# Kernel optimization log

Measured on AMD Instinct MI355X. Metric: run time of the kernel, lower is better.

## Reference

```python
import jax, jax.numpy as jnp
import numpy as np

S = 128          # voxel grid resolution per axis
NPB = 50000      # active voxels per batch element
B = 2            # batch size
C_IN = 64
C_OUT = 64
K = 3            # kernel size

# kernel offsets in [-1,0,1]^3, shape [27, 3]
_OFFS = np.stack(np.meshgrid(np.arange(-1, 2), np.arange(-1, 2), np.arange(-1, 2), indexing='ij'), axis=-1).reshape(-1, 3)


def setup_inputs() -> dict:
    rng = np.random.default_rng(0)
    coords_list = []
    for b in range(B):
        lin = rng.choice(S * S * S, size=NPB, replace=False)  # unique voxels
        x = lin // (S * S)
        y = (lin // S) % S
        z = lin % S
        coords_list.append(np.stack([np.full(NPB, b), x, y, z], axis=1))
    coords = jnp.asarray(np.concatenate(coords_list, axis=0), dtype=jnp.int32)  # [N,4]

    key = jax.random.key(0)
    k1, k2, k3 = jax.random.split(key, 3)
    feats = jax.random.normal(k1, (B * NPB, C_IN), dtype=jnp.float32)
    fan1 = C_IN * K ** 3
    fan2 = C_OUT * K ** 3
    W1 = jax.random.normal(k2, (K ** 3, C_IN, C_OUT), dtype=jnp.float32) / np.sqrt(fan1)
    W2 = jax.random.normal(k3, (K ** 3, C_OUT, C_OUT), dtype=jnp.float32) / np.sqrt(fan2)
    return {"feats": feats, "coords": coords, "W1": W1, "W2": W2}


def _encode(coords):
    # linear key: ((b*S + x)*S + y)*S + z ; fits in int32 for S=128, B small
    b, x, y, z = coords[:, 0], coords[:, 1], coords[:, 2], coords[:, 3]
    return ((b * S + x) * S + y) * S + z


def _sparse_conv(feats, coords, W):
    """Stride-1 sparse (submanifold-style) 3D conv: output coords == input coords.
    feats [N,Cin], coords [N,4], W [27,Cin,Cout] -> [N,Cout]."""
    N = feats.shape[0]
    keys = _encode(coords)
    order = jnp.argsort(keys)
    skeys = keys[order]
    offs = jnp.asarray(_OFFS, dtype=jnp.int32)  # [27,3]

    def gather_one(d):
        qxyz = coords[:, 1:4] + d[None, :]
        valid = jnp.all((qxyz >= 0) & (qxyz < S), axis=1)
        qkey = keys + (d[0] * S * S + d[1] * S + d[2])
        idx = jnp.clip(jnp.searchsorted(skeys, qkey), 0, N - 1)
        found = valid & (skeys[idx] == qkey)
        return jnp.where(found[:, None], feats[order[idx]], 0.0)  # [N,Cin]

    gathered = jax.vmap(gather_one)(offs)  # [27, N, Cin]
    return jnp.einsum('onc,ocd->nd', gathered, W)


def reference(feats, coords, W1, W2):
    h = _sparse_conv(feats, coords, W1)
    out = _sparse_conv(h, coords, W2)
    return out
```

## Files before the change

### kernel.cpp

```cpp
#include <hip/hip_runtime.h>
#include <stdint.h>

#define SGRID 128
#define CAP 4096

typedef _Float16 f16;
typedef f16 f16x8 __attribute__((ext_vector_type(8)));
typedef float f32x4 __attribute__((ext_vector_type(4)));
typedef unsigned long long u64;

static __device__ __forceinline__ f32x4 mfma16(uint4 a, uint4 b, f32x4 c) {
    union { uint4 u; f16x8 v; } ua, ub;
    ua.u = a; ub.u = b;
    return __builtin_amdgcn_mfma_f32_16x16x32_f16(ua.v, ub.v, c, 0, 0, 0);
}

static __device__ __forceinline__ void split8(const float* v, uint4& hu, uint4& lu) {
    union { f16 h[8]; uint4 u; } hv, lv;
    #pragma unroll
    for (int j = 0; j < 8; ++j) {
        f16 h = (f16)v[j];
        hv.h[j] = h;
        lv.h[j] = (f16)(v[j] - (float)h);
    }
    hu = hv.u; lu = lv.u;
}

static __device__ __forceinline__ void center_body(
    const float* __restrict__ A, const f16* __restrict__ Wp,
    float* __restrict__ O, int N, int gw, int lane)
{
    const int r = lane & 15, lq = lane >> 4;
    const int p0 = gw * 32;

    const uint4* wb = (const uint4*)Wp + 13 * 512 + lane;
    uint4 b[2][4];
    #pragma unroll
    for (int ct = 0; ct < 4; ++ct)
        #pragma unroll
        for (int ks = 0; ks < 2; ++ks)
            b[ks][ct] = wb[(ct * 2 + ks) * 64];

    uint4 ah[2][2], al[2][2];
    #pragma unroll
    for (int rt = 0; rt < 2; ++rt) {
        int row = p0 + rt * 16 + r;
        #pragma unroll
        for (int ks = 0; ks < 2; ++ks) {
            float v[8];
            if (row < N) {
                float4 v0 = *(const float4*)(A + (size_t)row * 64 + ks * 32 + lq * 8);
                float4 v1 = *(const float4*)(A + (size_t)row * 64 + ks * 32 + lq * 8 + 4);
                v[0]=v0.x; v[1]=v0.y; v[2]=v0.z; v[3]=v0.w;
                v[4]=v1.x; v[5]=v1.y; v[6]=v1.z; v[7]=v1.w;
            } else {
                #pragma unroll
                for (int j = 0; j < 8; ++j) v[j] = 0.f;
            }
            split8(v, ah[rt][ks], al[rt][ks]);
        }
    }

    f32x4 acc[2][4];
    #pragma unroll
    for (int i = 0; i < 2; ++i)
        #pragma unroll
        for (int j = 0; j < 4; ++j) acc[i][j] = (f32x4){0.f, 0.f, 0.f, 0.f};

    #pragma unroll
    for (int ks = 0; ks < 2; ++ks)
        #pragma unroll
        for (int rt = 0; rt < 2; ++rt)
            #pragma unroll
            for (int ct = 0; ct < 4; ++ct) {
                acc[rt][ct] = mfma16(ah[rt][ks], b[ks][ct], acc[rt][ct]);
                acc[rt][ct] = mfma16(al[rt][ks], b[ks][ct], acc[rt][ct]);
            }

    #pragma unroll
    for (int rt = 0; rt < 2; ++rt)
        #pragma unroll
        for (int j = 0; j < 4; ++j) {
            int row = p0 + rt * 16 + lq * 4 + j;
            if (row < N) {
                #pragma unroll
                for (int ct = 0; ct < 4; ++ct)
                    O[(size_t)row * 64 + ct * 16 + r] = acc[rt][ct][j];
            }
        }
}

__global__ void clear_meta(uint4* __restrict__ bitmap4, int nwords4, int* __restrict__ cnt) {
    const int stride = gridDim.x * 256;
    for (int i = blockIdx.x * 256 + threadIdx.x; i < nwords4; i += stride)
        bitmap4[i] = (uint4){0, 0, 0, 0};
    if (blockIdx.x == 0 && threadIdx.x < 26) cnt[threadIdx.x * 16] = 0;
}

__global__ void __launch_bounds__(256) scatter_prep(
    const int* __restrict__ coords, int* __restrict__ table,
    unsigned* __restrict__ bitmap, int N, int scatB,
    const float* __restrict__ W1, const float* __restrict__ W2,
    f16* __restrict__ Wp1, f16* __restrict__ Wp2)
{
    const int tid = threadIdx.x;
    if (blockIdx.x < scatB) {
        int i = blockIdx.x * 256 + tid;
        if (i < N) {
            int4 c = ((const int4*)coords)[i];
            int key = ((c.x * SGRID + c.y) * SGRID + c.z) * SGRID + c.w;
            table[key] = i;
            atomicOr(&bitmap[key >> 5], 1u << (key & 31));
        }
        return;
    }
    int idx = (blockIdx.x - scatB) * 256 + tid;
    const int half = 27 * 512;
    const float* W = (idx < half) ? W1 : W2;
    f16* Wp = (idx < half) ? Wp1 : Wp2;
    int id = (idx < half) ? idx : idx - half;
    int lane = id & 63;
    int ks = (id >> 6) & 1;
    int ct = (id >> 7) & 3;
    int o  = id >> 9;
    int co  = ct * 16 + (lane & 15);
    int ci0 = ks * 32 + (lane >> 4) * 8;
    union { f16 h[8]; uint4 u; } hv;
    #pragma unroll
    for (int j = 0; j < 8; ++j)
        hv.h[j] = (f16)W[((size_t)o * 64 + ci0 + j) * 64 + co];
    ((uint4*)Wp)[id] = hv.u;
}

__global__ void __launch_bounds__(256) build(
    const int* __restrict__ coords, const int* __restrict__ table,
    const unsigned* __restrict__ bitmap,
    int* __restrict__ pin, int* __restrict__ pout, int* __restrict__ cnt, int N)
{
    __shared__ u64 sbal[26][4];
    __shared__ int sbase4[26][4];

    const int tid = threadIdx.x, lane = tid & 63, wave = tid >> 6;
    const int n = blockIdx.x * 256 + tid;
    const bool valid = n < N;

    int4 c = {0, 0, 0, 0};
    if (valid) c = ((const int4*)coords)[n];
    const int z  = c.w;
    const int zb = (z == 0) ? 0 : z - 1;
    const int wofs = zb >> 5, sh = zb & 31;

    unsigned omask = 0;
    #pragma unroll
    for (int cidx = 0; cidx < 9; ++cidx) {
        int dx = cidx / 3 - 1, dy = cidx % 3 - 1;
        int qx = c.y + dx, qy = c.z + dy;
        bool colok = valid && ((unsigned)qx < SGRID) && ((unsigned)qy < SGRID);
        int colbase = ((c.x * SGRID + qx) * SGRID + qy) << 2;
        int wi = colok ? (colbase + wofs) : 0;
        unsigned w0 = bitmap[wi];
        unsigned w1 = bitmap[wi + 1];
        u64 w = (u64)w0 | ((u64)w1 << 32);
        unsigned t = (unsigned)(w >> sh) & 7u;
        if (z == 0)         t = (t << 1) & 6u;
        if (z == SGRID - 1) t &= 3u;
        t = colok ? t : 0u;
        omask |= t << (cidx * 3);
    }
    omask &= ~(1u << 13);

    #pragma unroll
    for (int s = 0; s < 26; ++s) {
        int o = s < 13 ? s : s + 1;
        u64 bal = __ballot((omask >> o) & 1u);
        if (lane == 0) sbal[s][wave] = bal;
    }
    __syncthreads();

    if (tid < 26) {
        int c0 = (int)__popcll(sbal[tid][0]);
        int c1 = (int)__popcll(sbal[tid][1]);
        int c2 = (int)__popcll(sbal[tid][2]);
        int c3 = (int)__popcll(sbal[tid][3]);
        int tot = c0 + c1 + c2 + c3;
        int base = tot ? atomicAdd(&cnt[tid * 16], tot) : 0;
        sbase4[tid][0] = base;
        sbase4[tid][1] = base + c0;
        sbase4[tid][2] = base + c0 + c1;
        sbase4[tid][3] = base + c0 + c1 + c2;
    }
    __syncthreads();

    const int key = ((c.x * SGRID + c.y) * SGRID + c.z) * SGRID + z;
    const u64 ltmask = (1ull << lane) - 1ull;
    unsigned m = omask;
    while (m) {
        int o = __ffs(m) - 1;
        m &= m - 1;
        int s = o - (o > 13 ? 1 : 0);
        int dx = o / 9 - 1;
        int r9 = o - (dx + 1) * 9;
        int dy = r9 / 3 - 1;
        int dz = r9 - (dy + 1) * 3 - 1;
        int qkey = key + dx * SGRID * SGRID + dy * SGRID + dz;
        int v = table[qkey];
        int pos = sbase4[s][wave] + (int)__popcll(sbal[s][wave] & ltmask);
        if (pos < CAP) {
            pin[s * CAP + pos]  = v;
            pout[s * CAP + pos] = n;
        }
    }
}

__global__ void __launch_bounds__(256) conv_center(
    const float* __restrict__ A, const f16* __restrict__ Wp,
    float* __restrict__ O, int N)
{
    int gw = (blockIdx.x * 256 + threadIdx.x) >> 6;
    if (gw < (N + 31) >> 5)
        center_body(A, Wp, O, N, gw, threadIdx.x & 63);
}

__global__ void __launch_bounds__(256) conv_sparse(
    const float* __restrict__ A, const f16* __restrict__ Wp,
    const int* __restrict__ pin, const int* __restrict__ pout,
    const int* __restrict__ cnt, float* __restrict__ O)
{
    int w = (blockIdx.x * 256 + threadIdx.x) >> 6;
    if (w >= 26 * 512) return;
    int slot  = w >> 9;
    int rem   = w & 511;
    int chunk = rem >> 1;
    int ch    = rem & 1;
    int cn = cnt[slot * 16]; if (cn > CAP) cn = CAP;
    int i0 = chunk * 16;
    if (i0 >= cn) return;
    int o = slot < 13 ? slot : slot + 1;
    const int lane = threadIdx.x & 63, r = lane & 15, lq = lane >> 4;

    const uint4* wb = (const uint4*)Wp + (size_t)o * 512 + lane;
    uint4 b[2][2];
    #pragma unroll
    for (int ct = 0; ct < 2; ++ct)
        #pragma unroll
        for (int ks = 0; ks < 2; ++ks)
            b[ct][ks] = wb[((ch * 2 + ct) * 2 + ks) * 64];

    int p = i0 + r;
    int in = (p < cn) ? pin[slot * CAP + p] : -1;
    uint4 ah[2], al[2];
    #pragma unroll
    for (int ks = 0; ks < 2; ++ks) {
        float v[8];
        if (in >= 0) {
            float4 v0 = *(const float4*)(A + (size_t)in * 64 + ks * 32 + lq * 8);
            float4 v1 = *(const float4*)(A + (size_t)in * 64 + ks * 32 + lq * 8 + 4);
            v[0]=v0.x; v[1]=v0.y; v[2]=v0.z; v[3]=v0.w;
            v[4]=v1.x; v[5]=v1.y; v[6]=v1.z; v[7]=v1.w;
        } else {
            #pragma unroll
            for (int j = 0; j < 8; ++j) v[j] = 0.f;
        }
        split8(v, ah[ks], al[ks]);
    }

    f32x4 acc[2];
    acc[0] = (f32x4){0.f, 0.f, 0.f, 0.f};
    acc[1] = (f32x4){0.f, 0.f, 0.f, 0.f};
    #pragma unroll
    for (int ks = 0; ks < 2; ++ks)
        #pragma unroll
        for (int ct = 0; ct < 2; ++ct) {
            acc[ct] = mfma16(ah[ks], b[ct][ks], acc[ct]);
            acc[ct] = mfma16(al[ks], b[ct][ks], acc[ct]);
        }

    #pragma unroll
    for (int j = 0; j < 4; ++j) {
        int pr = i0 + lq * 4 + j;
        if (pr < cn) {
            int oidx = pout[slot * CAP + pr];
            #pragma unroll
            for (int ct = 0; ct < 2; ++ct)
                atomicAdd(&O[(size_t)oidx * 64 + (ch * 2 + ct) * 16 + r], acc[ct][j]);
        }
    }
}

extern "C" void kernel_launch(void* const* d_in, const int* in_sizes, int n_in,
                              void* d_out, int out_size, void* d_ws, size_t ws_size,
                              hipStream_t stream) {
    const float* feats  = (const float*)d_in[0];
    const int*   coords = (const int*)d_in[1];
    const float* W1     = (const float*)d_in[2];
    const float* W2     = (const float*)d_in[3];
    float* out = (float*)d_out;

    const int N = in_sizes[0] / 64;
    const size_t nvox = 2ull * SGRID * SGRID * SGRID;

    char* p = (char*)d_ws;
    int*      table  = (int*)p;      p += nvox * 4;
    unsigned* bitmap = (unsigned*)p; p += (nvox / 32) * 4;
    p += 16;
    int*      cnt    = (int*)p;      p += 26 * 16 * 4;
    int*      pin    = (int*)p;      p += 26ull * CAP * 4;
    int*      pout   = (int*)p;      p += 26ull * CAP * 4;
    float*    H      = (float*)p;    p += (size_t)N * 64 * 4;
    f16*      Wp1    = (f16*)p;      p += 27ull * 4096 * 2;
    f16*      Wp2    = (f16*)p;      p += 27ull * 4096 * 2;

    const int bm4     = (int)(nvox / 32 / 4) + 1;
    const int scatB   = (N + 255) / 256;
    const int ngroups = (N + 31) / 32;
    const int centerB = (ngroups + 3) / 4;
    const int sparseB = 26 * 512 / 4;

    clear_meta<<<128, 256, 0, stream>>>((uint4*)bitmap, bm4, cnt);
    scatter_prep<<<scatB + 108, 256, 0, stream>>>(coords, table, bitmap, N, scatB,
                                                  W1, W2, Wp1, Wp2);
    build<<<scatB, 256, 0, stream>>>(coords, table, bitmap, pin, pout, cnt, N);
    conv_center<<<centerB, 256, 0, stream>>>(feats, Wp1, H, N);
    conv_sparse<<<sparseB, 256, 0, stream>>>(feats, Wp1, pin, pout, cnt, H);
    conv_center<<<centerB, 256, 0, stream>>>(H, Wp2, out, N);
    conv_sparse<<<sparseB, 256, 0, stream>>>(H, Wp2, pin, pout, cnt, out);
}
```

Measured before the change: 100.9 us.

## Pre-split input features to fp16 hi/lo and fuse center conv into build

```diff
diff --git a/kernel.cpp b/kernel.cpp
--- a/kernel.cpp
+++ b/kernel.cpp
@@ -24,6 +24,65 @@
         lv.h[j] = (f16)(v[j] - (float)h);
     }
     hu = hv.u; lu = lv.u;
+}
+
+static __device__ __forceinline__ void center_body_split(
+    const f16* __restrict__ Fp, const f16* __restrict__ Wp,
+    float* __restrict__ O, int N, int gw, int lane)
+{
+    const int r = lane & 15, lq = lane >> 4;
+    const int p0 = gw * 32;
+    const uint4* Fp4 = (const uint4*)Fp;
+
+    const uint4* wb = (const uint4*)Wp + 13 * 512 + lane;
+    uint4 b[2][4];
+    #pragma unroll
+    for (int ct = 0; ct < 4; ++ct)
+        #pragma unroll
+        for (int ks = 0; ks < 2; ++ks)
+            b[ks][ct] = wb[(ct * 2 + ks) * 64];
+
+    uint4 ah[2][2], al[2][2];
+    #pragma unroll
+    for (int rt = 0; rt < 2; ++rt) {
+        int row = p0 + rt * 16 + r;
+        if (row < N) {
+            size_t base = (size_t)row * 16;
+            ah[rt][0] = Fp4[base + lq];     ah[rt][1] = Fp4[base + 4 + lq];
+            al[rt][0] = Fp4[base + 8 + lq]; al[rt][1] = Fp4[base + 12 + lq];
+        } else {
+            ah[rt][0] = ah[rt][1] = (uint4){0,0,0,0};
+            al[rt][0] = al[rt][1] = (uint4){0,0,0,0};
+        }
+    }
+
+    f32x4 acc[2][4];
+    #pragma unroll
+    for (int i = 0; i < 2; ++i)
+        #pragma unroll
+        for (int j = 0; j < 4; ++j) acc[i][j] = (f32x4){0.f, 0.f, 0.f, 0.f};
+
+    #pragma unroll
+    for (int ks = 0; ks < 2; ++ks)
+        #pragma unroll
+        for (int rt = 0; rt < 2; ++rt)
+            #pragma unroll
+            for (int ct = 0; ct < 4; ++ct) {
+                acc[rt][ct] = mfma16(ah[rt][ks], b[ks][ct], acc[rt][ct]);
+                acc[rt][ct] = mfma16(al[rt][ks], b[ks][ct], acc[rt][ct]);
+            }
+
+    #pragma unroll
+    for (int rt = 0; rt < 2; ++rt)
+        #pragma unroll
+        for (int j = 0; j < 4; ++j) {
+            int row = p0 + rt * 16 + lq * 4 + j;
+            if (row < N) {
+                #pragma unroll
+                for (int ct = 0; ct < 4; ++ct)
+                    O[(size_t)row * 64 + ct * 16 + r] = acc[rt][ct][j];
+            }
+        }
 }
 
 static __device__ __forceinline__ void center_body(
@@ -101,11 +160,13 @@
     const int* __restrict__ coords, int* __restrict__ table,
     unsigned* __restrict__ bitmap, int N, int scatB,
     const float* __restrict__ W1, const float* __restrict__ W2,
-    f16* __restrict__ Wp1, f16* __restrict__ Wp2)
+    f16* __restrict__ Wp1, f16* __restrict__ Wp2,
+    const float* __restrict__ F, f16* __restrict__ Fp)
 {
     const int tid = threadIdx.x;
-    if (blockIdx.x < scatB) {
-        int i = blockIdx.x * 256 + tid;
+    int bid = blockIdx.x;
+    if (bid < scatB) {
+        int i = bid * 256 + tid;
         if (i < N) {
             int4 c = ((const int4*)coords)[i];
             int key = ((c.x * SGRID + c.y) * SGRID + c.z) * SGRID + c.w;
@@ -114,34 +175,64 @@
         }
         return;
     }
-    int idx = (blockIdx.x - scatB) * 256 + tid;
-    const int half = 27 * 512;
-    const float* W = (idx < half) ? W1 : W2;
-    f16* Wp = (idx < half) ? Wp1 : Wp2;
-    int id = (idx < half) ? idx : idx - half;
-    int lane = id & 63;
-    int ks = (id >> 6) & 1;
-    int ct = (id >> 7) & 3;
-    int o  = id >> 9;
-    int co  = ct * 16 + (lane & 15);
-    int ci0 = ks * 32 + (lane >> 4) * 8;
-    union { f16 h[8]; uint4 u; } hv;
-    #pragma unroll
-    for (int j = 0; j < 8; ++j)
-        hv.h[j] = (f16)W[((size_t)o * 64 + ci0 + j) * 64 + co];
-    ((uint4*)Wp)[id] = hv.u;
-}
-
-__global__ void __launch_bounds__(256) build(
+    bid -= scatB;
+    if (bid < 108) {
+        int idx = bid * 256 + tid;
+        const int half = 27 * 512;
+        const float* W = (idx < half) ? W1 : W2;
+        f16* Wp = (idx < half) ? Wp1 : Wp2;
+        int id = (idx < half) ? idx : idx - half;
+        int lane = id & 63;
+        int ks = (id >> 6) & 1;
+        int ct = (id >> 7) & 3;
+        int o  = id >> 9;
+        int co  = ct * 16 + (lane & 15);
+        int ci0 = ks * 32 + (lane >> 4) * 8;
+        union { f16 h[8]; uint4 u; } hv;
+        #pragma unroll
+        for (int j = 0; j < 8; ++j)
+            hv.h[j] = (f16)W[((size_t)o * 64 + ci0 + j) * 64 + co];
+        ((uint4*)Wp)[id] = hv.u;
+        return;
+    }
+    bid -= 108;
+    {
+        int i = bid * 256 + tid;
+        if (i * 8 < N * 64) {
+            float4 v0 = ((const float4*)F)[i * 2];
+            float4 v1 = ((const float4*)F)[i * 2 + 1];
+            float vv[8] = {v0.x, v0.y, v0.z, v0.w, v1.x, v1.y, v1.z, v1.w};
+            uint4 hu, lu;
+            split8(vv, hu, lu);
+            int n = i >> 3, c = (i & 7) * 8;
+            *(uint4*)(Fp + (size_t)n * 128 + c)      = hu;
+            *(uint4*)(Fp + (size_t)n * 128 + 64 + c) = lu;
+        }
+    }
+}
+
+__global__ void __launch_bounds__(256) build_center(
     const int* __restrict__ coords, const int* __restrict__ table,
     const unsigned* __restrict__ bitmap,
-    int* __restrict__ pin, int* __restrict__ pout, int* __restrict__ cnt, int N)
-{
+    int* __restrict__ pin, int* __restrict__ pout, int* __restrict__ cnt,
+    int N, int probeChunks,
+    const f16* __restrict__ Fp, const f16* __restrict__ Wp, float* __restrict__ H)
+{
+    const int tid = threadIdx.x;
+    const int bid = blockIdx.x;
+
+    if (bid >= probeChunks) {
+        int gw = ((bid - probeChunks) * 256 + tid) >> 6;
+        if (gw < (N + 31) >> 5)
+            center_body_split(Fp, Wp, H, N, gw, tid & 63);
+        return;
+    }
+
     __shared__ u64 sbal[26][4];
     __shared__ int sbase4[26][4];
 
-    const int tid = threadIdx.x, lane = tid & 63, wave = tid >> 6;
-    const int n = blockIdx.x * 256 + tid;
+    const int lane = tid & 63, wave = tid >> 6;
+    const int n = bid * 256 + tid;
     const bool valid = n < N;
 
     int4 c = {0, 0, 0, 0};
@@ -221,8 +312,8 @@
         center_body(A, Wp, O, N, gw, threadIdx.x & 63);
 }
 
-__global__ void __launch_bounds__(256) conv_sparse(
-    const float* __restrict__ A, const f16* __restrict__ Wp,
+__global__ void __launch_bounds__(256) conv_sparse_split(
+    const f16* __restrict__ Fp, const f16* __restrict__ Wp,
     const int* __restrict__ pin, const int* __restrict__ pout,
     const int* __restrict__ cnt, float* __restrict__ O)
 {
@@ -237,6 +328,67 @@
     if (i0 >= cn) return;
     int o = slot < 13 ? slot : slot + 1;
     const int lane = threadIdx.x & 63, r = lane & 15, lq = lane >> 4;
+    const uint4* Fp4 = (const uint4*)Fp;
+
+    const uint4* wb = (const uint4*)Wp + (size_t)o * 512 + lane;
+    uint4 b[2][2];
+    #pragma unroll
+    for (int ct = 0; ct < 2; ++ct)
+        #pragma unroll
+        for (int ks = 0; ks < 2; ++ks)
+            b[ct][ks] = wb[((ch * 2 + ct) * 2 + ks) * 64];
+
+    int p = i0 + r;
+    int in = (p < cn) ? pin[slot * CAP + p] : -1;
+    uint4 ah[2], al[2];
+    if (in >= 0) {
+        size_t base = (size_t)in * 16;
+        ah[0] = Fp4[base + lq];     ah[1] = Fp4[base + 4 + lq];
+        al[0] = Fp4[base + 8 + lq]; al[1] = Fp4[base + 12 + lq];
+    } else {
+        ah[0] = ah[1] = (uint4){0,0,0,0};
+        al[0] = al[1] = (uint4){0,0,0,0};
+    }
+
+    f32x4 acc[2];
+    acc[0] = (f32x4){0.f, 0.f, 0.f, 0.f};
+    acc[1] = (f32x4){0.f, 0.f, 0.f, 0.f};
+    #pragma unroll
+    for (int ks = 0; ks < 2; ++ks)
+        #pragma unroll
+        for (int ct = 0; ct < 2; ++ct) {
+            acc[ct] = mfma16(ah[ks], b[ct][ks], acc[ct]);
+            acc[ct] = mfma16(al[ks], b[ct][ks], acc[ct]);
+        }
+
+    #pragma unroll
+    for (int j = 0; j < 4; ++j) {
+        int pr = i0 + lq * 4 + j;
+        if (pr < cn) {
+            int oidx = pout[slot * CAP + pr];
+            #pragma unroll
+            for (int ct = 0; ct < 2; ++ct)
+                atomicAdd(&O[(size_t)oidx * 64 + (ch * 2 + ct) * 16 + r], acc[ct][j]);
+        }
+    }
+}
+
+__global__ void __launch_bounds__(256) conv_sparse(
+    const float* __restrict__ A, const f16* __restrict__ Wp,
+    const int* __restrict__ pin, const int* __restrict__ pout,
+    const int* __restrict__ cnt, float* __restrict__ O)
+{
+    int w = (blockIdx.x * 256 + threadIdx.x) >> 6;
+    if (w >= 26 * 512) return;
+    int slot  = w >> 9;
+    int rem   = w & 511;
+    int chunk = rem >> 1;
+    int ch    = rem & 1;
+    int cn = cnt[slot * 16]; if (cn > CAP) cn = CAP;
+    int i0 = chunk * 16;
+    if (i0 >= cn) return;
+    int o = slot < 13 ? slot : slot + 1;
+    const int lane = threadIdx.x & 63, r = lane & 15, lq = lane >> 4;
 
     const uint4* wb = (const uint4*)Wp + (size_t)o * 512 + lane;
     uint4 b[2][2];
@@ -307,21 +459,24 @@
     int*      pin    = (int*)p;      p += 26ull * CAP * 4;
     int*      pout   = (int*)p;      p += 26ull * CAP * 4;
     float*    H      = (float*)p;    p += (size_t)N * 64 * 4;
+    f16*      Fp     = (f16*)p;      p += (size_t)N * 128 * 2;
     f16*      Wp1    = (f16*)p;      p += 27ull * 4096 * 2;
     f16*      Wp2    = (f16*)p;      p += 27ull * 4096 * 2;
 
     const int bm4     = (int)(nvox / 32 / 4) + 1;
     const int scatB   = (N + 255) / 256;
+    const int splitB  = (N * 64 / 8 + 255) / 256;
     const int ngroups = (N + 31) / 32;
     const int centerB = (ngroups + 3) / 4;
     const int sparseB = 26 * 512 / 4;
 
-    clear_meta<<<128, 256, 0, stream>>>((uint4*)bitmap, bm4, cnt);
-    scatter_prep<<<scatB + 108, 256, 0, stream>>>(coords, table, bitmap, N, scatB,
-                                                  W1, W2, Wp1, Wp2);
-    build<<<scatB, 256, 0, stream>>>(coords, table, bitmap, pin, pout, cnt, N);
-    conv_center<<<centerB, 256, 0, stream>>>(feats, Wp1, H, N);
-    conv_sparse<<<sparseB, 256, 0, stream>>>(feats, Wp1, pin, pout, cnt, H);
+    clear_meta<<<256, 256, 0, stream>>>((uint4*)bitmap, bm4, cnt);
+    scatter_prep<<<scatB + 108 + splitB, 256, 0, stream>>>(coords, table, bitmap, N, scatB,
+                                                           W1, W2, Wp1, Wp2, feats, Fp);
+    build_center<<<scatB + centerB, 256, 0, stream>>>(coords, table, bitmap,
+                                                      pin, pout, cnt, N, scatB,
+                                                      Fp, Wp1, H);
+    conv_sparse_split<<<sparseB, 256, 0, stream>>>(Fp, Wp1, pin, pout, cnt, H);
     conv_center<<<centerB, 256, 0, stream>>>(H, Wp2, out, N);
     conv_sparse<<<sparseB, 256, 0, stream>>>(H, Wp2, pin, pout, cnt, out);
 }
```

After: 101.3 us. No clear change (+0.4%).

## Fuse neighbor search and all 27 offsets into one output-stationary conv kernel

Applied to the files above, without the earlier changes.

```diff
diff --git a/kernel.cpp b/kernel.cpp
--- a/kernel.cpp
+++ b/kernel.cpp
@@ -2,7 +2,6 @@
 #include <stdint.h>
 
 #define SGRID 128
-#define CAP 4096
 
 typedef _Float16 f16;
 typedef f16 f16x8 __attribute__((ext_vector_type(8)));
@@ -26,75 +25,10 @@
     hu = hv.u; lu = lv.u;
 }
 
-static __device__ __forceinline__ void center_body(
-    const float* __restrict__ A, const f16* __restrict__ Wp,
-    float* __restrict__ O, int N, int gw, int lane)
-{
-    const int r = lane & 15, lq = lane >> 4;
-    const int p0 = gw * 32;
-
-    const uint4* wb = (const uint4*)Wp + 13 * 512 + lane;
-    uint4 b[2][4];
-    #pragma unroll
-    for (int ct = 0; ct < 4; ++ct)
-        #pragma unroll
-        for (int ks = 0; ks < 2; ++ks)
-            b[ks][ct] = wb[(ct * 2 + ks) * 64];
-
-    uint4 ah[2][2], al[2][2];
-    #pragma unroll
-    for (int rt = 0; rt < 2; ++rt) {
-        int row = p0 + rt * 16 + r;
-        #pragma unroll
-        for (int ks = 0; ks < 2; ++ks) {
-            float v[8];
-            if (row < N) {
-                float4 v0 = *(const float4*)(A + (size_t)row * 64 + ks * 32 + lq * 8);
-                float4 v1 = *(const float4*)(A + (size_t)row * 64 + ks * 32 + lq * 8 + 4);
-                v[0]=v0.x; v[1]=v0.y; v[2]=v0.z; v[3]=v0.w;
-                v[4]=v1.x; v[5]=v1.y; v[6]=v1.z; v[7]=v1.w;
-            } else {
-                #pragma unroll
-                for (int j = 0; j < 8; ++j) v[j] = 0.f;
-            }
-            split8(v, ah[rt][ks], al[rt][ks]);
-        }
-    }
-
-    f32x4 acc[2][4];
-    #pragma unroll
-    for (int i = 0; i < 2; ++i)
-        #pragma unroll
-        for (int j = 0; j < 4; ++j) acc[i][j] = (f32x4){0.f, 0.f, 0.f, 0.f};
-
-    #pragma unroll
-    for (int ks = 0; ks < 2; ++ks)
-        #pragma unroll
-        for (int rt = 0; rt < 2; ++rt)
-            #pragma unroll
-            for (int ct = 0; ct < 4; ++ct) {
-                acc[rt][ct] = mfma16(ah[rt][ks], b[ks][ct], acc[rt][ct]);
-                acc[rt][ct] = mfma16(al[rt][ks], b[ks][ct], acc[rt][ct]);
-            }
-
-    #pragma unroll
-    for (int rt = 0; rt < 2; ++rt)
-        #pragma unroll
-        for (int j = 0; j < 4; ++j) {
-            int row = p0 + rt * 16 + lq * 4 + j;
-            if (row < N) {
-                #pragma unroll
-                for (int ct = 0; ct < 4; ++ct)
-                    O[(size_t)row * 64 + ct * 16 + r] = acc[rt][ct][j];
-            }
-        }
-}
-
-__global__ void clear_meta(uint4* __restrict__ bitmap4, int nwords4, int* __restrict__ cnt) {
+__global__ void clear_meta(uint4* __restrict__ bitmap4, int nwords4) {
     const int stride = gridDim.x * 256;
     for (int i = blockIdx.x * 256 + threadIdx.x; i < nwords4; i += stride)
         bitmap4[i] = (uint4){0, 0, 0, 0};
-    if (blockIdx.x == 0 && threadIdx.x < 26) cnt[threadIdx.x * 16] = 0;
 }
 
 __global__ void __launch_bounds__(256) scatter_prep(
@@ -132,159 +66,119 @@
     ((uint4*)Wp)[id] = hv.u;
 }
 
-__global__ void __launch_bounds__(256) build(
+__global__ void __launch_bounds__(256) conv(
+    const float* __restrict__ A, const f16* __restrict__ Wp,
     const int* __restrict__ coords, const int* __restrict__ table,
-    const unsigned* __restrict__ bitmap,
-    int* __restrict__ pin, int* __restrict__ pout, int* __restrict__ cnt, int N)
+    const unsigned* __restrict__ bitmap, unsigned* __restrict__ omaskArr,
+    float* __restrict__ O, int N, int probe)
 {
-    __shared__ u64 sbal[26][4];
-    __shared__ int sbase4[26][4];
-
-    const int tid = threadIdx.x, lane = tid & 63, wave = tid >> 6;
-    const int n = blockIdx.x * 256 + tid;
-    const bool valid = n < N;
+    const int w = (blockIdx.x * 256 + threadIdx.x) >> 6;
+    const int ngroups = (N + 31) >> 5;
+    if (w >= ngroups) return;
+    const int lane = threadIdx.x & 63;
+    const int r = lane & 15, lq = lane >> 4;
+    const int p0 = w * 32;
+    const int n  = p0 + lane;
+    const bool owner = (lane < 32) && (n < N);
 
     int4 c = {0, 0, 0, 0};
-    if (valid) c = ((const int4*)coords)[n];
-    const int z  = c.w;
-    const int zb = (z == 0) ? 0 : z - 1;
-    const int wofs = zb >> 5, sh = zb & 31;
-
-    unsigned omask = 0;
-    #pragma unroll
-    for (int cidx = 0; cidx < 9; ++cidx) {
-        int dx = cidx / 3 - 1, dy = cidx % 3 - 1;
-        int qx = c.y + dx, qy = c.z + dy;
-        bool colok = valid && ((unsigned)qx < SGRID) && ((unsigned)qy < SGRID);
-        int colbase = ((c.x * SGRID + qx) * SGRID + qy) << 2;
-        int wi = colok ? (colbase + wofs) : 0;
-        unsigned w0 = bitmap[wi];
-        unsigned w1 = bitmap[wi + 1];
-        u64 w = (u64)w0 | ((u64)w1 << 32);
-        unsigned t = (unsigned)(w >> sh) & 7u;
-        if (z == 0)         t = (t << 1) & 6u;
-        if (z == SGRID - 1) t &= 3u;
-        t = colok ? t : 0u;
-        omask |= t << (cidx * 3);
-    }
-    omask &= ~(1u << 13);
-
-    #pragma unroll
-    for (int s = 0; s < 26; ++s) {
-        int o = s < 13 ? s : s + 1;
-        u64 bal = __ballot((omask >> o) & 1u);
-        if (lane == 0) sbal[s][wave] = bal;
-    }
-    __syncthreads();
-
-    if (tid < 26) {
-        int c0 = (int)__popcll(sbal[tid][0]);
-        int c1 = (int)__popcll(sbal[tid][1]);
-        int c2 = (int)__popcll(sbal[tid][2]);
-        int c3 = (int)__popcll(sbal[tid][3]);
-        int tot = c0 + c1 + c2 + c3;
-        int base = tot ? atomicAdd(&cnt[tid * 16], tot) : 0;
-        sbase4[tid][0] = base;
-        sbase4[tid][1] = base + c0;
-        sbase4[tid][2] = base + c0 + c1;
-        sbase4[tid][3] = base + c0 + c1 + c2;
-    }
-    __syncthreads();
-
-    const int key = ((c.x * SGRID + c.y) * SGRID + c.z) * SGRID + z;
-    const u64 ltmask = (1ull << lane) - 1ull;
-    unsigned m = omask;
-    while (m) {
-        int o = __ffs(m) - 1;
-        m &= m - 1;
-        int s = o - (o > 13 ? 1 : 0);
-        int dx = o / 9 - 1;
-        int r9 = o - (dx + 1) * 9;
-        int dy = r9 / 3 - 1;
-        int dz = r9 - (dy + 1) * 3 - 1;
-        int qkey = key + dx * SGRID * SGRID + dy * SGRID + dz;
-        int v = table[qkey];
-        int pos = sbase4[s][wave] + (int)__popcll(sbal[s][wave] & ltmask);
-        if (pos < CAP) {
-            pin[s * CAP + pos]  = v;
-            pout[s * CAP + pos] = n;
-        }
-    }
-}
-
-__global__ void __launch_bounds__(256) conv_center(
-    const float* __restrict__ A, const f16* __restrict__ Wp,
-    float* __restrict__ O, int N)
-{
-    int gw = (blockIdx.x * 256 + threadIdx.x) >> 6;
-    if (gw < (N + 31) >> 5)
-        center_body(A, Wp, O, N, gw, threadIdx.x & 63);
-}
-
-__global__ void __launch_bounds__(256) conv_sparse(
-    const float* __restrict__ A, const f16* __restrict__ Wp,
-    const int* __restrict__ pin, const int* __restrict__ pout,
-    const int* __restrict__ cnt, float* __restrict__ O)
-{
-    int w = (blockIdx.x * 256 + threadIdx.x) >> 6;
-    if (w >= 26 * 512) return;
-    int slot  = w >> 9;
-    int rem   = w & 511;
-    int chunk = rem >> 1;
-    int ch    = rem & 1;
-    int cn = cnt[slot * 16]; if (cn > CAP) cn = CAP;
-    int i0 = chunk * 16;
-    if (i0 >= cn) return;
-    int o = slot < 13 ? slot : slot + 1;
-    const int lane = threadIdx.x & 63, r = lane & 15, lq = lane >> 4;
-
-    const uint4* wb = (const uint4*)Wp + (size_t)o * 512 + lane;
-    uint4 b[2][2];
-    #pragma unroll
-    for (int ct = 0; ct < 2; ++ct)
-        #pragma unroll
-        for (int ks = 0; ks < 2; ++ks)
-            b[ct][ks] = wb[((ch * 2 + ct) * 2 + ks) * 64];
-
-    int p = i0 + r;
-    int in = (p < cn) ? pin[slot * CAP + p] : -1;
-    uint4 ah[2], al[2];
-    #pragma unroll
-    for (int ks = 0; ks < 2; ++ks) {
-        float v[8];
-        if (in >= 0) {
-            float4 v0 = *(const float4*)(A + (size_t)in * 64 + ks * 32 + lq * 8);
-            float4 v1 = *(const float4*)(A + (size_t)in * 64 + ks * 32 + lq * 8 + 4);
-            v[0]=v0.x; v[1]=v0.y; v[2]=v0.z; v[3]=v0.w;
-            v[4]=v1.x; v[5]=v1.y; v[6]=v1.z; v[7]=v1.w;
-        } else {
+    if (owner) c = ((const int4*)coords)[n];
+    const int key = ((c.x * SGRID + c.y) * SGRID + c.z) * SGRID + c.w;
+
+    unsigned om = 0;
+    if (probe) {
+        if (owner) {
+            const int z = c.w;
+            const int zb = (z == 0) ? 0 : z - 1;
+            const int wofs = zb >> 5, sh = zb & 31;
             #pragma unroll
-            for (int j = 0; j < 8; ++j) v[j] = 0.f;
-        }
-        split8(v, ah[ks], al[ks]);
-    }
-
-    f32x4 acc[2];
-    acc[0] = (f32x4){0.f, 0.f, 0.f, 0.f};
-    acc[1] = (f32x4){0.f, 0.f, 0.f, 0.f};
-    #pragma unroll
-    for (int ks = 0; ks < 2; ++ks)
-        #pragma unroll
-        for (int ct = 0; ct < 2; ++ct) {
-            acc[ct] = mfma16(ah[ks], b[ct][ks], acc[ct]);
-            acc[ct] = mfma16(al[ks], b[ct][ks], acc[ct]);
-        }
-
-    #pragma unroll
-    for (int j = 0; j < 4; ++j) {
-        int pr = i0 + lq * 4 + j;
-        if (pr < cn) {
-            int oidx = pout[slot * CAP + pr];
+            for (int cidx = 0; cidx < 9; ++cidx) {
+                int dx = cidx / 3 - 1, dy = cidx % 3 - 1;
+                int qx = c.y + dx, qy = c.z + dy;
+                bool colok = ((unsigned)qx < SGRID) && ((unsigned)qy < SGRID);
+                int wi = colok ? ((((c.x * SGRID + qx) * SGRID + qy) << 2) + wofs) : 0;
+                unsigned w0 = bitmap[wi];
+                unsigned w1 = bitmap[wi + 1];
+                u64 wnd = (u64)w0 | ((u64)w1 << 32);
+                unsigned t = (unsigned)(wnd >> sh) & 7u;
+                if (z == 0)         t = (t << 1) & 6u;
+                if (z == SGRID - 1) t &= 3u;
+                t = colok ? t : 0u;
+                om |= t << (cidx * 3);
+            }
+            omaskArr[n] = om;
+        }
+    } else {
+        if (owner) om = omaskArr[n];
+    }
+
+    f32x4 acc[2][4];
+    #pragma unroll
+    for (int i = 0; i < 2; ++i)
+        #pragma unroll
+        for (int j = 0; j < 4; ++j) acc[i][j] = (f32x4){0.f, 0.f, 0.f, 0.f};
+
+    const uint4* Wb = (const uint4*)Wp;
+
+    #pragma unroll 1
+    for (int o = 0; o < 27; ++o) {
+        u64 bal = __ballot((om >> o) & 1u);
+        if (!bal) continue;
+
+        int nbr_l = -1;
+        if ((om >> o) & 1u) {
+            int dkey = (o / 9 - 1) * SGRID * SGRID + ((o / 3) % 3 - 1) * SGRID + (o % 3 - 1);
+            nbr_l = table[key + dkey];
+        }
+        int nb0 = __shfl(nbr_l, r);
+        int nb1 = __shfl(nbr_l, r + 16);
+
+        uint4 b[4][2];
+        #pragma unroll
+        for (int ct = 0; ct < 4; ++ct)
             #pragma unroll
-            for (int ct = 0; ct < 2; ++ct)
-                atomicAdd(&O[(size_t)oidx * 64 + (ch * 2 + ct) * 16 + r], acc[ct][j]);
-        }
-    }
+            for (int ks = 0; ks < 2; ++ks)
+                b[ct][ks] = Wb[o * 512 + (ct * 2 + ks) * 64 + lane];
+
+        #pragma unroll
+        for (int rt = 0; rt < 2; ++rt) {
+            u64 rtm = rt ? (bal & 0xFFFF0000ull) : (bal & 0xFFFFull);
+            if (!rtm) continue;
+            int nb = rt ? nb1 : nb0;
+            uint4 ah[2], al[2];
+            if (nb >= 0) {
+                #pragma unroll
+                for (int ks = 0; ks < 2; ++ks) {
+                    float4 v0 = *(const float4*)(A + (size_t)nb * 64 + ks * 32 + lq * 8);
+                    float4 v1 = *(const float4*)(A + (size_t)nb * 64 + ks * 32 + lq * 8 + 4);
+                    float v[8] = {v0.x, v0.y, v0.z, v0.w, v1.x, v1.y, v1.z, v1.w};
+                    split8(v, ah[ks], al[ks]);
+                }
+            } else {
+                ah[0] = ah[1] = (uint4){0,0,0,0};
+                al[0] = al[1] = (uint4){0,0,0,0};
+            }
+            #pragma unroll
+            for (int ks = 0; ks < 2; ++ks)
+                #pragma unroll
+                for (int ct = 0; ct < 4; ++ct) {
+                    acc[rt][ct] = mfma16(ah[ks], b[ct][ks], acc[rt][ct]);
+                    acc[rt][ct] = mfma16(al[ks], b[ct][ks], acc[rt][ct]);
+                }
+        }
+    }
+
+    #pragma unroll
+    for (int rt = 0; rt < 2; ++rt)
+        #pragma unroll
+        for (int j = 0; j < 4; ++j) {
+            int row = p0 + rt * 16 + lq * 4 + j;
+            if (row < N) {
+                #pragma unroll
+                for (int ct = 0; ct < 4; ++ct)
+                    O[(size_t)row * 64 + ct * 16 + r] = acc[rt][ct][j];
+            }
+        }
 }
 
 extern "C" void kernel_launch(void* const* d_in, const int* in_sizes, int n_in,
@@ -303,9 +197,7 @@
     int*      table  = (int*)p;      p += nvox * 4;
     unsigned* bitmap = (unsigned*)p; p += (nvox / 32) * 4;
     p += 16;
-    int*      cnt    = (int*)p;      p += 26 * 16 * 4;
-    int*      pin    = (int*)p;      p += 26ull * CAP * 4;
-    int*      pout   = (int*)p;      p += 26ull * CAP * 4;
+    unsigned* omaskA = (unsigned*)p; p += (size_t)N * 4;
     float*    H      = (float*)p;    p += (size_t)N * 64 * 4;
     f16*      Wp1    = (f16*)p;      p += 27ull * 4096 * 2;
     f16*      Wp2    = (f16*)p;      p += 27ull * 4096 * 2;
@@ -313,15 +205,11 @@
     const int bm4     = (int)(nvox / 32 / 4) + 1;
     const int scatB   = (N + 255) / 256;
     const int ngroups = (N + 31) / 32;
-    const int centerB = (ngroups + 3) / 4;
-    const int sparseB = 26 * 512 / 4;
-
-    clear_meta<<<128, 256, 0, stream>>>((uint4*)bitmap, bm4, cnt);
+    const int convB   = (ngroups + 3) / 4;
+
+    clear_meta<<<256, 256, 0, stream>>>((uint4*)bitmap, bm4);
     scatter_prep<<<scatB + 108, 256, 0, stream>>>(coords, table, bitmap, N, scatB,
                                                   W1, W2, Wp1, Wp2);
-    build<<<scatB, 256, 0, stream>>>(coords, table, bitmap, pin, pout, cnt, N);
-    conv_center<<<centerB, 256, 0, stream>>>(feats, Wp1, H, N);
-    conv_sparse<<<sparseB, 256, 0, stream>>>(feats, Wp1, pin, pout, cnt, H);
-    conv_center<<<centerB, 256, 0, stream>>>(H, Wp2, out, N);
-    conv_sparse<<<sparseB, 256, 0, stream>>>(H, Wp2, pin, pout, cnt, out);
-}
+    conv<<<convB, 256, 0, stream>>>(feats, Wp1, coords, table, bitmap, omaskA, H,   N, 1);
+    conv<<<convB, 256, 0, stream>>>(H,     Wp2, coords, table, bitmap, omaskA, out, N, 0);
+}
```

After: 100.2 us. Within noise of the previous version (-0.7%).

## Fuse first center conv into prep kernel and batch neighbor table lookups

Applied to the files above, without the earlier changes.

```diff
diff --git a/kernel.cpp b/kernel.cpp
--- a/kernel.cpp
+++ b/kernel.cpp
@@ -26,20 +26,12 @@
     hu = hv.u; lu = lv.u;
 }
 
-static __device__ __forceinline__ void center_body(
-    const float* __restrict__ A, const f16* __restrict__ Wp,
+static __device__ __forceinline__ void center_tail(
+    const float* __restrict__ A, const uint4 b[2][4],
     float* __restrict__ O, int N, int gw, int lane)
 {
     const int r = lane & 15, lq = lane >> 4;
     const int p0 = gw * 32;
-
-    const uint4* wb = (const uint4*)Wp + 13 * 512 + lane;
-    uint4 b[2][4];
-    #pragma unroll
-    for (int ct = 0; ct < 4; ++ct)
-        #pragma unroll
-        for (int ks = 0; ks < 2; ++ks)
-            b[ks][ct] = wb[(ct * 2 + ks) * 64];
 
     uint4 ah[2][2], al[2][2];
     #pragma unroll
@@ -97,15 +89,41 @@
     if (blockIdx.x == 0 && threadIdx.x < 26) cnt[threadIdx.x * 16] = 0;
 }
 
-__global__ void __launch_bounds__(256) scatter_prep(
-    const int* __restrict__ coords, int* __restrict__ table,
-    unsigned* __restrict__ bitmap, int N, int scatB,
-    const float* __restrict__ W1, const float* __restrict__ W2,
-    f16* __restrict__ Wp1, f16* __restrict__ Wp2)
+__global__ void __launch_bounds__(256) prep_center(
+    const float* __restrict__ F, const float* __restrict__ W1, float* __restrict__ H,
+    const int* __restrict__ coords, int* __restrict__ table, unsigned* __restrict__ bitmap,
+    const float* __restrict__ W2, f16* __restrict__ Wp1, f16* __restrict__ Wp2,
+    int N, int centerB, int scatB)
 {
     const int tid = threadIdx.x;
-    if (blockIdx.x < scatB) {
-        int i = blockIdx.x * 256 + tid;
+    int bid = blockIdx.x;
+
+    if (bid < centerB) {
+        int gw = (bid * 256 + tid) >> 6;
+        if (gw >= (N + 31) >> 5) return;
+        const int lane = tid & 63, r = lane & 15, lq = lane >> 4;
+        const float* Wc = W1 + 13 * 4096;
+        uint4 b[2][4];
+        #pragma unroll
+        for (int ct = 0; ct < 4; ++ct) {
+            int co = ct * 16 + r;
+            #pragma unroll
+            for (int ks = 0; ks < 2; ++ks) {
+                int ci0 = ks * 32 + lq * 8;
+                union { f16 h[8]; uint4 u; } hv;
+                #pragma unroll
+                for (int j = 0; j < 8; ++j)
+                    hv.h[j] = (f16)Wc[(ci0 + j) * 64 + co];
+                b[ks][ct] = hv.u;
+            }
+        }
+        center_tail(F, b, H, N, gw, lane);
+        return;
+    }
+    bid -= centerB;
+
+    if (bid < scatB) {
+        int i = bid * 256 + tid;
         if (i < N) {
             int4 c = ((const int4*)coords)[i];
             int key = ((c.x * SGRID + c.y) * SGRID + c.z) * SGRID + c.w;
@@ -114,22 +132,26 @@
         }
         return;
     }
-    int idx = (blockIdx.x - scatB) * 256 + tid;
-    const int half = 27 * 512;
-    const float* W = (idx < half) ? W1 : W2;
-    f16* Wp = (idx < half) ? Wp1 : Wp2;
-    int id = (idx < half) ? idx : idx - half;
-    int lane = id & 63;
-    int ks = (id >> 6) & 1;
-    int ct = (id >> 7) & 3;
-    int o  = id >> 9;
-    int co  = ct * 16 + (lane & 15);
-    int ci0 = ks * 32 + (lane >> 4) * 8;
-    union { f16 h[8]; uint4 u; } hv;
-    #pragma unroll
-    for (int j = 0; j < 8; ++j)
-        hv.h[j] = (f16)W[((size_t)o * 64 + ci0 + j) * 64 + co];
-    ((uint4*)Wp)[id] = hv.u;
+    bid -= scatB;
+
+    {
+        int idx = bid * 256 + tid;
+        const int half = 27 * 512;
+        const float* W = (idx < half) ? W1 : W2;
+        f16* Wp = (idx < half) ? Wp1 : Wp2;
+        int id = (idx < half) ? idx : idx - half;
+        int lane = id & 63;
+        int ks = (id >> 6) & 1;
+        int ct = (id >> 7) & 3;
+        int o  = id >> 9;
+        int co  = ct * 16 + (lane & 15);
+        int ci0 = ks * 32 + (lane >> 4) * 8;
+        union { f16 h[8]; uint4 u; } hv;
+        #pragma unroll
+        for (int j = 0; j < 8; ++j)
+            hv.h[j] = (f16)W[((size_t)o * 64 + ci0 + j) * 64 + co];
+        ((uint4*)Wp)[id] = hv.u;
+    }
 }
 
 __global__ void __launch_bounds__(256) build(
@@ -156,8 +178,7 @@
         int dx = cidx / 3 - 1, dy = cidx % 3 - 1;
         int qx = c.y + dx, qy = c.z + dy;
         bool colok = valid && ((unsigned)qx < SGRID) && ((unsigned)qy < SGRID);
-        int colbase = ((c.x * SGRID + qx) * SGRID + qy) << 2;
-        int wi = colok ? (colbase + wofs) : 0;
+        int wi = colok ? ((((c.x * SGRID + qx) * SGRID + qy) << 2) + wofs) : 0;
         unsigned w0 = bitmap[wi];
         unsigned w1 = bitmap[wi + 1];
         u64 w = (u64)w0 | ((u64)w1 << 32);
@@ -169,10 +190,20 @@
     }
     omask &= ~(1u << 13);
 
+    const int key = ((c.x * SGRID + c.y) * SGRID + c.z) * SGRID + z;
+    int nb[26];
     #pragma unroll
     for (int s = 0; s < 26; ++s) {
         int o = s < 13 ? s : s + 1;
-        u64 bal = __ballot((omask >> o) & 1u);
+        bool occ = (omask >> o) & 1u;
+        int qkey = key + (o / 9 - 1) * SGRID * SGRID + ((o / 3) % 3 - 1) * SGRID + (o % 3 - 1);
+        int v = table[occ ? qkey : 0];
+        nb[s] = occ ? v : -1;
+    }
+
+    #pragma unroll
+    for (int s = 0; s < 26; ++s) {
+        u64 bal = __ballot(nb[s] >= 0);
         if (lane == 0) sbal[s][wave] = bal;
     }
     __syncthreads();
@@ -191,23 +222,15 @@
     }
     __syncthreads();
 
-    const int key = ((c.x * SGRID + c.y) * SGRID + c.z) * SGRID + z;
     const u64 ltmask = (1ull << lane) - 1ull;
-    unsigned m = omask;
-    while (m) {
-        int o = __ffs(m) - 1;
-        m &= m - 1;
-        int s = o - (o > 13 ? 1 : 0);
-        int dx = o / 9 - 1;
-        int r9 = o - (dx + 1) * 9;
-        int dy = r9 / 3 - 1;
-        int dz = r9 - (dy + 1) * 3 - 1;
-        int qkey = key + dx * SGRID * SGRID + dy * SGRID + dz;
-        int v = table[qkey];
-        int pos = sbase4[s][wave] + (int)__popcll(sbal[s][wave] & ltmask);
-        if (pos < CAP) {
-            pin[s * CAP + pos]  = v;
-            pout[s * CAP + pos] = n;
+    #pragma unroll
+    for (int s = 0; s < 26; ++s) {
+        if (nb[s] >= 0) {
+            int pos = sbase4[s][wave] + (int)__popcll(sbal[s][wave] & ltmask);
+            if (pos < CAP) {
+                pin[s * CAP + pos]  = nb[s];
+                pout[s * CAP + pos] = n;
+            }
         }
     }
 }
@@ -217,8 +240,16 @@
     float* __restrict__ O, int N)
 {
     int gw = (blockIdx.x * 256 + threadIdx.x) >> 6;
-    if (gw < (N + 31) >> 5)
-        center_body(A, Wp, O, N, gw, threadIdx.x & 63);
+    if (gw >= (N + 31) >> 5) return;
+    const int lane = threadIdx.x & 63;
+    const uint4* wb = (const uint4*)Wp + 13 * 512 + lane;
+    uint4 b[2][4];
+    #pragma unroll
+    for (int ct = 0; ct < 4; ++ct)
+        #pragma unroll
+        for (int ks = 0; ks < 2; ++ks)
+            b[ks][ct] = wb[(ct * 2 + ks) * 64];
+    center_tail(A, b, O, N, gw, lane);
 }
 
 __global__ void __launch_bounds__(256) conv_sparse(
@@ -316,11 +347,10 @@
     const int centerB = (ngroups + 3) / 4;
     const int sparseB = 26 * 512 / 4;
 
-    clear_meta<<<128, 256, 0, stream>>>((uint4*)bitmap, bm4, cnt);
-    scatter_prep<<<scatB + 108, 256, 0, stream>>>(coords, table, bitmap, N, scatB,
-                                                  W1, W2, Wp1, Wp2);
+    clear_meta<<<256, 256, 0, stream>>>((uint4*)bitmap, bm4, cnt);
+    prep_center<<<centerB + scatB + 108, 256, 0, stream>>>(
+        feats, W1, H, coords, table, bitmap, W2, Wp1, Wp2, N, centerB, scatB);
     build<<<scatB, 256, 0, stream>>>(coords, table, bitmap, pin, pout, cnt, N);
-    conv_center<<<centerB, 256, 0, stream>>>(feats, Wp1, H, N);
     conv_sparse<<<sparseB, 256, 0, stream>>>(feats, Wp1, pin, pout, cnt, H);
     conv_center<<<centerB, 256, 0, stream>>>(H, Wp2, out, N);
     conv_sparse<<<sparseB, 256, 0, stream>>>(H, Wp2, pin, pout, cnt, out);
```

New measurement: 99.26 us. Within noise of the previous version (-1.7%).
